# Optimization experiments

Hardware: AMD Instinct MI355X
Metric: run time of the kernel (lower is better)

The kernel has to match this reference:

```python
import jax, jax.numpy as jnp
import numpy as np

B, D, H, E, K = 8192, 1024, 256, 16, 4


def setup_inputs() -> dict:
    key = jax.random.key(0)
    ks = jax.random.split(key, 6)
    s_d = D ** -0.5
    s_h = H ** -0.5
    return {
        "x": jax.random.normal(ks[0], (B, D), dtype=jnp.float32),
        "route_w": jax.random.normal(ks[1], (E, D), dtype=jnp.float32) * s_d,
        "w1": jax.random.normal(ks[2], (E, H, D), dtype=jnp.float32) * s_d,
        "b1": jax.random.normal(ks[3], (E, H), dtype=jnp.float32) * s_d,
        "w2": jax.random.normal(ks[4], (E, D, H), dtype=jnp.float32) * s_h,
        "b2": jax.random.normal(ks[5], (E, D), dtype=jnp.float32) * s_h,
    }


def _moe_forward(x, route_w, w1, b1, w2, b2):
    # Router: logits (B, E) -> top-k softmax weights scattered back to (B, E).
    logits = x @ route_w.T
    top_vals, top_idx = jax.lax.top_k(logits, K)
    top_w = jax.nn.softmax(top_vals, axis=-1)
    rows = jnp.arange(x.shape[0])[:, None]
    weights = jnp.zeros_like(logits).at[rows, top_idx].set(top_w)  # (B, E)

    # Experts: out = sum_e w[:, e] * relu(relu(x W1e^T + b1e) W2e^T + b2e)
    # Non-selected experts have weight 0, so dense-then-weight matches the
    # original masked gather/scatter math exactly (dropout = 0).
    def step(out, params_e):
        W1, bb1, W2, bb2, we = params_e
        h = jax.nn.relu(x @ W1.T + bb1)       # (B, H)
        y = jax.nn.relu(h @ W2.T + bb2)       # (B, D)
        return out + y * we[:, None], None

    out0 = jnp.zeros_like(x)
    out, _ = jax.lax.scan(step, out0, (w1, b1, w2, b2, weights.T))
    return out


def reference(x, route_w, w1, b1, w2, b2):
    return _moe_forward(x, route_w, w1, b1, w2, b2)
```

## Files before the change

### kernel.cpp

```cpp
#include <hip/hip_runtime.h>
#include <stdint.h>

typedef unsigned short u16;
typedef __attribute__((ext_vector_type(8))) short bf16x8;
typedef __attribute__((ext_vector_type(4))) float f32x4;
typedef __attribute__((ext_vector_type(8))) u16 u16x8;
typedef __attribute__((ext_vector_type(4))) u16 u16x4;

#define NTOK 8192
#define DDIM 1024
#define HDIM 256
#define NEXP 16
#define MAXT 272
#define MAXMT (MAXT * 2)
#define MAXSLOT (MAXT * 128)

__device__ __forceinline__ u16 f2bf(float f) {
  uint32_t u = __builtin_bit_cast(uint32_t, f);
  u += 0x7FFFu + ((u >> 16) & 1u);
  return (u16)(u >> 16);
}
__device__ __forceinline__ float bf2f(u16 h) {
  return __builtin_bit_cast(float, (uint32_t)h << 16);
}

__device__ __forceinline__ void gll16(const void* g, void* l) {
  __builtin_amdgcn_global_load_lds((const __attribute__((address_space(1))) void*)g,
                                   (__attribute__((address_space(3))) void*)l,
                                   16, 0, 0);
}

__global__ __launch_bounds__(256) void cvt2_kernel(const float* __restrict__ a,
                                                   const float* __restrict__ b,
                                                   u16* __restrict__ oa,
                                                   u16* __restrict__ ob,
                                                   int nba) {
  const float* in; u16* out;
  int bx = blockIdx.x;
  if (bx < nba) { in = a; out = oa; } else { in = b; out = ob; bx -= nba; }
  size_t i = ((size_t)bx * 256 + threadIdx.x) * 8;
  const float4 p = *(const float4*)(in + i);
  const float4 q = *(const float4*)(in + i + 4);
  u16x8 o;
  o[0] = f2bf(p.x); o[1] = f2bf(p.y); o[2] = f2bf(p.z); o[3] = f2bf(p.w);
  o[4] = f2bf(q.x); o[5] = f2bf(q.y); o[6] = f2bf(q.z); o[7] = f2bf(q.w);
  *(u16x8*)(out + i) = o;
}

__global__ __launch_bounds__(256) void zero_out_kernel(float* __restrict__ p) {
  size_t i = ((size_t)blockIdx.x * 256 + threadIdx.x) * 4;
  *(float4*)(p + i) = (float4){0.f, 0.f, 0.f, 0.f};
}

__global__ __launch_bounds__(256) void router_kernel(const float* __restrict__ x,
                                                     const float* __restrict__ rw,
                                                     int* __restrict__ epack,
                                                     float* __restrict__ ew,
                                                     u16* __restrict__ xbf) {
  __shared__ __align__(16) uint8_t rwlds[65536];
  const int tid = threadIdx.x;

#pragma unroll
  for (int i = 0; i < 16; ++i) {
    int byte = (i * 256 + tid) * 16;
    int sw = byte ^ (((byte >> 8) & 7) << 4);
    *(float4*)(rwlds + sw) = *(const float4*)((const uint8_t*)rw + byte);
  }
  __syncthreads();

  const int lane = tid & 63, wid = tid >> 6;
  const int s = lane & 15;
  const int tok = blockIdx.x * 16 + wid * 4 + (lane >> 4);
  const float* xrow = x + (size_t)tok * DDIM;
  u16* xbrow = xbf + (size_t)tok * DDIM;

  double acc[NEXP];
#pragma unroll
  for (int e = 0; e < NEXP; ++e) acc[e] = 0.0;

#pragma unroll 4
  for (int g = 0; g < 16; ++g) {
    const int d = s * 64 + g * 4;
    float4 xv = *(const float4*)(xrow + d);
    u16x4 o;
    o[0] = f2bf(xv.x); o[1] = f2bf(xv.y); o[2] = f2bf(xv.z); o[3] = f2bf(xv.w);
    *(u16x4*)(xbrow + d) = o;
    const double x0 = xv.x, x1 = xv.y, x2 = xv.z, x3 = xv.w;
    const int roff = (s * 256 + g * 16) ^ ((s & 7) << 4);
#pragma unroll
    for (int e = 0; e < NEXP; ++e) {
      float4 rv = *(const float4*)(rwlds + e * 4096 + roff);
      acc[e] = fma(x0, (double)rv.x, acc[e]);
      acc[e] = fma(x1, (double)rv.y, acc[e]);
      acc[e] = fma(x2, (double)rv.z, acc[e]);
      acc[e] = fma(x3, (double)rv.w, acc[e]);
    }
  }

#define FOLD(H, M)                                                   \
  _Pragma("unroll") for (int i = 0; i < H; ++i) {                    \
    double send = (lane & M) ? acc[i] : acc[i + H];                  \
    double recv = __shfl_xor(send, M);                               \
    acc[i] = ((lane & M) ? acc[i + H] : acc[i]) + recv;              \
  }
  FOLD(8, 1)
  FOLD(4, 2)
  FOLD(2, 4)
  FOLD(1, 8)
#undef FOLD
  const int e_mine = ((lane & 1) << 3) | ((lane & 2) << 1) |
                     ((lane & 4) >> 1) | ((lane & 8) >> 3);

  double val = acc[0];
  double tv[4]; int tidx[4];
#pragma unroll
  for (int k = 0; k < 4; ++k) {
    double bv = val; int be = e_mine;
#pragma unroll
    for (int m = 1; m < 16; m <<= 1) {
      double ov = __shfl_xor(bv, m);
      int oe = __shfl_xor(be, m);
      if (ov > bv || (ov == bv && oe < be)) { bv = ov; be = oe; }
    }
    tv[k] = bv; tidx[k] = be;
    if (e_mine == be) val = -1.0e300;
  }

  if ((lane & 15) == 0) {
    float m0 = (float)tv[0];
    float w[4]; float sum = 0.f;
#pragma unroll
    for (int k = 0; k < 4; ++k) { w[k] = expf((float)tv[k] - m0); sum += w[k]; }
    epack[tok] = tidx[0] | (tidx[1] << 8) | (tidx[2] << 16) | (tidx[3] << 24);
#pragma unroll
    for (int k = 0; k < 4; ++k) ew[tok * 4 + k] = w[k] / sum;
  }
}

__global__ __launch_bounds__(1024) void compact_kernel(const int* __restrict__ epack,
                                                       const float* __restrict__ ew,
                                                       int* __restrict__ texp,
                                                       int* __restrict__ perm,
                                                       float* __restrict__ wsl,
                                                       int* __restrict__ islot) {
  __shared__ int wave_cnt[16][NEXP];
  __shared__ int counts_sm[NEXP];
  __shared__ int wtot[16], wave_off[16];
  const int e = blockIdx.x;
  const int tid = threadIdx.x, lane = tid & 63, w = tid >> 6;

  int ep[8]; unsigned m[8];
#pragma unroll
  for (int j = 0; j < 8; ++j) {
    ep[j] = epack[tid * 8 + j];
    m[j] = (1u << (ep[j] & 255)) | (1u << ((ep[j] >> 8) & 255)) |
           (1u << ((ep[j] >> 16) & 255)) | (1u << ((ep[j] >> 24) & 255));
  }
#pragma unroll
  for (int ee = 0; ee < NEXP; ++ee) {
    int c = 0;
#pragma unroll
    for (int j = 0; j < 8; ++j) c += (m[j] >> ee) & 1u;
#pragma unroll
    for (int off = 32; off > 0; off >>= 1) c += __shfl_xor(c, off);
    if (lane == 0) wave_cnt[w][ee] = c;
  }
  unsigned fm = 0;
#pragma unroll
  for (int j = 0; j < 8; ++j) fm |= ((m[j] >> e) & 1u) << j;
  int s = __popc(fm);
  int incl = s;
#pragma unroll
  for (int d = 1; d < 64; d <<= 1) {
    int t2 = __shfl_up(incl, d);
    if (lane >= d) incl += t2;
  }
  if (lane == 63) wtot[w] = incl;
  __syncthreads();
  if (tid < NEXP) {
    int c = 0;
    for (int w2 = 0; w2 < 16; ++w2) c += wave_cnt[w2][tid];
    counts_sm[tid] = c;
  }
  if (tid == 0) {
    int run = 0;
    for (int w2 = 0; w2 < 16; ++w2) { wave_off[w2] = run; run += wtot[w2]; }
  }
  __syncthreads();
  int base = 0;
  for (int ee = 0; ee < NEXP; ++ee)
    if (ee < e) base += ((counts_sm[ee] + 127) >> 7) << 7;
  int pos = base + wave_off[w] + (incl - s);
#pragma unroll
  for (int j = 0; j < 8; ++j) {
    if ((fm >> j) & 1u) {
      int tok = tid * 8 + j;
      int b0 = ep[j] & 255, b1 = (ep[j] >> 8) & 255, b2_ = (ep[j] >> 16) & 255;
      int k = (b0 == e) ? 0 : ((b1 == e) ? 1 : ((b2_ == e) ? 2 : 3));
      perm[pos] = tok;
      wsl[pos] = ew[tok * 4 + k];
      islot[tok * 4 + k] = pos;
      ++pos;
    }
  }
  int cnt = counts_sm[e];
  int pad = (((cnt + 127) >> 7) << 7) - cnt;
  if (tid < pad) { perm[base + cnt + tid] = 0; wsl[base + cnt + tid] = 0.f; }
  if (e == 0 && tid == 0) {
    int tc = 0;
    for (int ee = 0; ee < NEXP; ++ee) {
      int nt = (counts_sm[ee] + 127) >> 7;
      for (int i = 0; i < nt; ++i) texp[tc++] = ee;
    }
    for (; tc < MAXT; ++tc) texp[tc] = -1;
  }
}

__device__ __forceinline__ void stage128(const u16* __restrict__ base, int ld,
                                         int kbase, uint8_t* dst, int tid) {
#pragma unroll
  for (int i = 0; i < 4; ++i) {
    int u = i * 256 + tid;
    int row = u >> 3, g = u & 7;
    gll16(base + (size_t)row * ld + kbase + ((g ^ (row & 7)) << 3), dst + u * 16);
  }
}
__device__ __forceinline__ void stage64(const u16* __restrict__ base, int ld,
                                        int kbase, uint8_t* dst, int tid) {
#pragma unroll
  for (int i = 0; i < 2; ++i) {
    int u = i * 256 + tid;
    int row = u >> 3, g = u & 7;
    gll16(base + (size_t)row * ld + kbase + ((g ^ (row & 7)) << 3), dst + u * 16);
  }
}
__device__ __forceinline__ void stage_gather64(const u16* __restrict__ xbf,
                                               const int tok[2], int kbase,
                                               uint8_t* dst, int tid) {
#pragma unroll
  for (int i = 0; i < 2; ++i) {
    int u = i * 256 + tid;
    int g = u & 7;
    gll16(xbf + (size_t)tok[i] * DDIM + kbase + ((g ^ ((u >> 3) & 7)) << 3), dst + u * 16);
  }
}

__device__ __forceinline__ void mma64(const uint8_t* Ab, const uint8_t* Bb,
                                      f32x4 acc[2][4], int wm, int wn,
                                      int lrow, int lk) {
#pragma unroll
  for (int s = 0; s < 2; ++s) {
    bf16x8 af[2], bfr[4];
#pragma unroll
    for (int f = 0; f < 2; ++f) {
      int ar = wm * 32 + f * 16 + lrow;
      af[f] = *(const bf16x8*)(Ab + ar * 128 + ((((s << 2) | lk) ^ (ar & 7)) << 4));
    }
#pragma unroll
    for (int f = 0; f < 4; ++f) {
      int br = wn * 64 + f * 16 + lrow;
      bfr[f] = *(const bf16x8*)(Bb + br * 128 + ((((s << 2) | lk) ^ (br & 7)) << 4));
    }
#pragma unroll
    for (int i = 0; i < 2; ++i)
#pragma unroll
      for (int j = 0; j < 4; ++j)
        acc[i][j] = __builtin_amdgcn_mfma_f32_16x16x32_bf16(af[i], bfr[j], acc[i][j], 0, 0, 0);
  }
}

__global__ __launch_bounds__(256) void gemm1_kernel(const u16* __restrict__ xbf,
                                                    const u16* __restrict__ w1bf,
                                                    const float* __restrict__ b1,
                                                    const int* __restrict__ texp,
                                                    const int* __restrict__ perm,
                                                    u16* __restrict__ Hc, int mt0) {
  __shared__ __align__(16) uint8_t smem[2][24576];
  const int mt = mt0 + blockIdx.x;
  const int e = (mt < MAXMT) ? texp[mt >> 1] : -1;
  if (e < 0) return;
  const int n0 = blockIdx.y * 128;
  const int tid = threadIdx.x;
  const int lane = tid & 63, wid = tid >> 6;
  const int wm = wid >> 1, wn = wid & 1;
  const int lrow = lane & 15, lk = lane >> 4;

  int tok[2];
#pragma unroll
  for (int i = 0; i < 2; ++i) tok[i] = perm[mt * 64 + ((i * 256 + tid) >> 3)];
  const u16* Bsrc = w1bf + ((size_t)e * HDIM + n0) * DDIM;

  f32x4 acc[2][4];
#pragma unroll
  for (int i = 0; i < 2; ++i)
#pragma unroll
    for (int j = 0; j < 4; ++j) acc[i][j] = (f32x4){0.f, 0.f, 0.f, 0.f};

  stage_gather64(xbf, tok, 0, smem[0], tid);
  stage128(Bsrc, DDIM, 0, smem[0] + 8192, tid);
  __syncthreads();
  int cur = 0;
  for (int kt = 0; kt < 16; ++kt) {
    if (kt < 15) {
      stage_gather64(xbf, tok, (kt + 1) * 64, smem[cur ^ 1], tid);
      stage128(Bsrc, DDIM, (kt + 1) * 64, smem[cur ^ 1] + 8192, tid);
    }
    mma64(smem[cur], smem[cur] + 8192, acc, wm, wn, lrow, lk);
    __syncthreads();
    cur ^= 1;
  }
#pragma unroll
  for (int j = 0; j < 4; ++j) {
    int n = n0 + wn * 64 + j * 16 + lrow;
    float bias = b1[e * HDIM + n];
#pragma unroll
    for (int i = 0; i < 2; ++i) {
      int rloc = (mt - mt0) * 64 + wm * 32 + i * 16 + lk * 4;
#pragma unroll
      for (int r = 0; r < 4; ++r) {
        float h = fmaxf(acc[i][j][r] + bias, 0.f);
        Hc[((size_t)rloc + r) * HDIM + n] = f2bf(h);
      }
    }
  }
}

__global__ __launch_bounds__(256) void gemm2_main_kernel(const u16* __restrict__ Hc,
                                                         const u16* __restrict__ w2bf,
                                                         const float* __restrict__ b2,
                                                         const int* __restrict__ texp,
                                                         u16* __restrict__ ybuf,
                                                         int nbase, int NC) {
  __shared__ __align__(16) uint8_t smem[2][24576];
  const int mt = blockIdx.x;
  const int e = texp[mt >> 1];
  if (e < 0) return;
  const int nl0 = blockIdx.y * 128;
  const int tid = threadIdx.x;
  const int lane = tid & 63, wid = tid >> 6;
  const int wm = wid >> 1, wn = wid & 1;
  const int lrow = lane & 15, lk = lane >> 4;

  const u16* Asrc = Hc + (size_t)mt * 64 * HDIM;
  const u16* Bsrc = w2bf + ((size_t)e * DDIM + nbase + nl0) * HDIM;

  f32x4 acc[2][4];
#pragma unroll
  for (int i = 0; i < 2; ++i)
#pragma unroll
    for (int j = 0; j < 4; ++j) acc[i][j] = (f32x4){0.f, 0.f, 0.f, 0.f};

  stage64(Asrc, HDIM, 0, smem[0], tid);
  stage128(Bsrc, HDIM, 0, smem[0] + 8192, tid);
  __syncthreads();
  int cur = 0;
  for (int kt = 0; kt < 4; ++kt) {
    if (kt < 3) {
      stage64(Asrc, HDIM, (kt + 1) * 64, smem[cur ^ 1], tid);
      stage128(Bsrc, HDIM, (kt + 1) * 64, smem[cur ^ 1] + 8192, tid);
    }
    mma64(smem[cur], smem[cur] + 8192, acc, wm, wn, lrow, lk);
    __syncthreads();
    cur ^= 1;
  }
  float bias[4];
#pragma unroll
  for (int j = 0; j < 4; ++j)
    bias[j] = b2[e * DDIM + nbase + nl0 + wn * 64 + j * 16 + lrow];
#pragma unroll
  for (int i = 0; i < 2; ++i) {
#pragma unroll
    for (int r = 0; r < 4; ++r) {
      int slot = mt * 64 + wm * 32 + i * 16 + lk * 4 + r;
#pragma unroll
      for (int j = 0; j < 4; ++j) {
        int nloc = nl0 + wn * 64 + j * 16 + lrow;
        float h = fmaxf(acc[i][j][r] + bias[j], 0.f);
        ybuf[(size_t)slot * NC + nloc] = f2bf(h);
      }
    }
  }
}

__global__ __launch_bounds__(256) void gemm2_fb_kernel(const u16* __restrict__ Hc,
                                                       const u16* __restrict__ w2bf,
                                                       const float* __restrict__ b2,
                                                       const int* __restrict__ texp,
                                                       const int* __restrict__ perm,
                                                       const float* __restrict__ wsl,
                                                       float* __restrict__ out, int mt0) {
  __shared__ __align__(16) uint8_t smem[2][24576];
  const int mt = mt0 + blockIdx.x;
  const int e = (mt < MAXMT) ? texp[mt >> 1] : -1;
  if (e < 0) return;
  const int nl0 = blockIdx.y * 128;
  const int tid = threadIdx.x;
  const int lane = tid & 63, wid = tid >> 6;
  const int wm = wid >> 1, wn = wid & 1;
  const int lrow = lane & 15, lk = lane >> 4;

  const u16* Asrc = Hc + (size_t)(mt - mt0) * 64 * HDIM;
  const u16* Bsrc = w2bf + ((size_t)e * DDIM + nl0) * HDIM;

  f32x4 acc[2][4];
#pragma unroll
  for (int i = 0; i < 2; ++i)
#pragma unroll
    for (int j = 0; j < 4; ++j) acc[i][j] = (f32x4){0.f, 0.f, 0.f, 0.f};

  stage64(Asrc, HDIM, 0, smem[0], tid);
  stage128(Bsrc, HDIM, 0, smem[0] + 8192, tid);
  __syncthreads();
  int cur = 0;
  for (int kt = 0; kt < 4; ++kt) {
    if (kt < 3) {
      stage64(Asrc, HDIM, (kt + 1) * 64, smem[cur ^ 1], tid);
      stage128(Bsrc, HDIM, (kt + 1) * 64, smem[cur ^ 1] + 8192, tid);
    }
    mma64(smem[cur], smem[cur] + 8192, acc, wm, wn, lrow, lk);
    __syncthreads();
    cur ^= 1;
  }
  float bias[4];
#pragma unroll
  for (int j = 0; j < 4; ++j)
    bias[j] = b2[e * DDIM + nl0 + wn * 64 + j * 16 + lrow];
#pragma unroll
  for (int i = 0; i < 2; ++i) {
#pragma unroll
    for (int r = 0; r < 4; ++r) {
      int slot = mt * 64 + wm * 32 + i * 16 + lk * 4 + r;
      int tokn = perm[slot];
      float w = wsl[slot];
#pragma unroll
      for (int j = 0; j < 4; ++j) {
        int n = nl0 + wn * 64 + j * 16 + lrow;
        float h = fmaxf(acc[i][j][r] + bias[j], 0.f);
        atomicAdd(&out[(size_t)tokn * DDIM + n], w * h);
      }
    }
  }
}

__global__ __launch_bounds__(256) void combine_kernel(const u16* __restrict__ ybuf,
                                                      const float* __restrict__ ew,
                                                      const int* __restrict__ islot,
                                                      float* __restrict__ out,
                                                      int n0, int NC, int cshift) {
  int gid = blockIdx.x * 256 + threadIdx.x;
  int t = gid >> cshift;
  int c = (gid & ((1 << cshift) - 1)) << 4;
  const int4 sl = *(const int4*)(islot + t * 4);
  const float4 w = *(const float4*)(ew + t * 4);
  float a[16];
#pragma unroll
  for (int k = 0; k < 16; ++k) a[k] = 0.f;
#define ACCROW(SL, W)                                                      \
  {                                                                        \
    u16x8 y0 = *(const u16x8*)(ybuf + (size_t)(SL)*NC + c);                \
    u16x8 y1 = *(const u16x8*)(ybuf + (size_t)(SL)*NC + c + 8);            \
    _Pragma("unroll") for (int k = 0; k < 8; ++k) {                        \
      a[k] += (W)*bf2f(y0[k]); a[8 + k] += (W)*bf2f(y1[k]);                \
    }                                                                      \
  }
  ACCROW(sl.x, w.x); ACCROW(sl.y, w.y); ACCROW(sl.z, w.z); ACCROW(sl.w, w.w);
#undef ACCROW
  float* o = out + (size_t)t * DDIM + n0 + c;
#pragma unroll
  for (int k = 0; k < 16; k += 4)
    *(float4*)(o + k) = (float4){a[k], a[k + 1], a[k + 2], a[k + 3]};
}

extern "C" void kernel_launch(void* const* d_in, const int* in_sizes, int n_in,
                              void* d_out, int out_size, void* d_ws, size_t ws_size,
                              hipStream_t stream) {
  const float* x = (const float*)d_in[0];
  const float* route_w = (const float*)d_in[1];
  const float* w1 = (const float*)d_in[2];
  const float* b1 = (const float*)d_in[3];
  const float* w2 = (const float*)d_in[4];
  const float* b2 = (const float*)d_in[5];
  float* out = (float*)d_out;

  uint8_t* ws = (uint8_t*)d_ws;
  const size_t OFF_EPACK = 0;
  const size_t OFF_EW    = 32768;
  const size_t OFF_ISLOT = 163840;
  const size_t OFF_TEXP  = 294912;
  const size_t OFF_PERM  = 296960;
  const size_t OFF_WSL   = 436224;
  const size_t OFF_X     = 1048576;
  const size_t OFF_W1    = OFF_X + (size_t)NTOK * DDIM * 2;
  const size_t OFF_W2    = OFF_W1 + (size_t)NEXP * HDIM * DDIM * 2;
  const size_t OFF_HC    = OFF_W2 + (size_t)NEXP * DDIM * HDIM * 2;
  const size_t OFF_Y     = OFF_HC + (size_t)MAXSLOT * HDIM * 2;

  int* epack  = (int*)(ws + OFF_EPACK);
  float* ew   = (float*)(ws + OFF_EW);
  int* islot  = (int*)(ws + OFF_ISLOT);
  int* texp   = (int*)(ws + OFF_TEXP);
  int* perm   = (int*)(ws + OFF_PERM);
  float* wsl  = (float*)(ws + OFF_WSL);
  u16* xbf    = (u16*)(ws + OFF_X);
  u16* w1bf   = (u16*)(ws + OFF_W1);
  u16* w2bf   = (u16*)(ws + OFF_W2);
  u16* Hc     = (u16*)(ws + OFF_HC);
  u16* ybuf   = (u16*)(ws + OFF_Y);

  const int nba = (NEXP * HDIM * DDIM) / 2048;
  cvt2_kernel<<<dim3(nba * 2), 256, 0, stream>>>(w1, w2, w1bf, w2bf, nba);
  router_kernel<<<dim3(NTOK / 16), 256, 0, stream>>>(x, route_w, epack, ew, xbf);
  compact_kernel<<<dim3(NEXP), 1024, 0, stream>>>(epack, ew, texp, perm, wsl, islot);

  int ybN = 0;
  for (int cand = 1024; cand >= 128; cand >>= 1) {
    if (ws_size >= OFF_Y + (size_t)MAXSLOT * cand * 2) { ybN = cand; break; }
  }

  if (ybN > 0) {
    gemm1_kernel<<<dim3(MAXMT, HDIM / 128), 256, 0, stream>>>(xbf, w1bf, b1, texp, perm, Hc, 0);
    int cshift = __builtin_ctz(ybN >> 4);
    for (int nb = 0; nb < DDIM; nb += ybN) {
      gemm2_main_kernel<<<dim3(MAXMT, ybN / 128), 256, 0, stream>>>(
          Hc, w2bf, b2, texp, ybuf, nb, ybN);
      combine_kernel<<<dim3((NTOK << cshift) / 256), 256, 0, stream>>>(
          ybuf, ew, islot, out, nb, ybN, cshift);
    }
  } else {
    long room = (long)ws_size - (long)OFF_HC;
    int CT = (int)(room / 65536);
    if (CT > MAXT) CT = MAXT;
    if (CT < 16) CT = 16;
    zero_out_kernel<<<dim3((NTOK * DDIM) / 1024), 256, 0, stream>>>(out);
    for (int t0 = 0; t0 < MAXT; t0 += CT) {
      int ct = (MAXT - t0 < CT) ? (MAXT - t0) : CT;
      gemm1_kernel<<<dim3(ct * 2, HDIM / 128), 256, 0, stream>>>(
          xbf, w1bf, b1, texp, perm, Hc, t0 * 2);
      gemm2_fb_kernel<<<dim3(ct * 2, DDIM / 128), 256, 0, stream>>>(
          Hc, w2bf, b2, texp, perm, wsl, out, t0 * 2);
    }
  }
}
```

Measured before the change: 141.6 us.

## Fuse expert GEMM1 and GEMM2 into one kernel keeping hidden tile in LDS

```diff
diff --git a/kernel.cpp b/kernel.cpp
--- a/kernel.cpp
+++ b/kernel.cpp
@@ -269,6 +269,103 @@
   }
 }
 
+__global__ __launch_bounds__(256) void fused_kernel(const u16* __restrict__ xbf,
+                                                    const u16* __restrict__ w1bf,
+                                                    const u16* __restrict__ w2bf,
+                                                    const float* __restrict__ b1,
+                                                    const float* __restrict__ b2,
+                                                    const int* __restrict__ texp,
+                                                    const int* __restrict__ perm,
+                                                    u16* __restrict__ ybuf, int NC) {
+  __shared__ __align__(16) uint8_t smem[81920];
+  const int mt = blockIdx.x;
+  const int e = texp[mt >> 1];
+  if (e < 0) return;
+  const int tid = threadIdx.x;
+  const int lane = tid & 63, wid = tid >> 6;
+  const int wm = wid >> 1, wn = wid & 1;
+  const int lrow = lane & 15, lk = lane >> 4;
+  uint8_t* stg = smem + 32768;
+
+  int tok[2];
+#pragma unroll
+  for (int i = 0; i < 2; ++i) tok[i] = perm[mt * 64 + ((i * 256 + tid) >> 3)];
+
+  f32x4 acc[2][4];
+#pragma unroll
+  for (int i = 0; i < 2; ++i)
+#pragma unroll
+    for (int j = 0; j < 4; ++j) acc[i][j] = (f32x4){0.f, 0.f, 0.f, 0.f};
+
+  for (int half = 0; half < 2; ++half) {
+    const u16* Bsrc = w1bf + ((size_t)e * HDIM + half * 128) * DDIM;
+    stage_gather64(xbf, tok, 0, stg, tid);
+    stage128(Bsrc, DDIM, 0, stg + 8192, tid);
+    __syncthreads();
+    int cur = 0;
+    for (int kt = 0; kt < 16; ++kt) {
+      if (kt < 15) {
+        stage_gather64(xbf, tok, (kt + 1) * 64, stg + ((cur ^ 1) * 24576), tid);
+        stage128(Bsrc, DDIM, (kt + 1) * 64, stg + ((cur ^ 1) * 24576) + 8192, tid);
+      }
+      mma64(stg + cur * 24576, stg + cur * 24576 + 8192, acc, wm, wn, lrow, lk);
+      __syncthreads();
+      cur ^= 1;
+    }
+#pragma unroll
+    for (int j = 0; j < 4; ++j) {
+      float bias = b1[e * HDIM + half * 128 + wn * 64 + j * 16 + lrow];
+      int g = j * 2 + (lrow >> 3);
+#pragma unroll
+      for (int i = 0; i < 2; ++i) {
+#pragma unroll
+        for (int r = 0; r < 4; ++r) {
+          int row = wm * 32 + i * 16 + lk * 4 + r;
+          float h = fmaxf(acc[i][j][r] + bias, 0.f);
+          int addr = (half * 2 + wn) * 8192 + row * 128 +
+                     ((g ^ (row & 7)) << 4) + (lrow & 7) * 2;
+          *(u16*)(smem + addr) = f2bf(h);
+          acc[i][j][r] = 0.f;
+        }
+      }
+    }
+  }
+  __syncthreads();
+
+  const u16* B2 = w2bf + (size_t)e * DDIM * HDIM;
+  stage128(B2, HDIM, 0, stg, tid);
+  __syncthreads();
+  int cur = 0;
+  for (int s = 0; s < 32; ++s) {
+    const int nb = s >> 2, kt = s & 3;
+    if (s < 31) {
+      const int nb2 = (s + 1) >> 2, kt2 = (s + 1) & 3;
+      stage128(B2 + (size_t)(nb2 * 128) * HDIM, HDIM, kt2 * 64,
+               stg + ((cur ^ 1) << 14), tid);
+    }
+    mma64(smem + kt * 8192, stg + (cur << 14), acc, wm, wn, lrow, lk);
+    if (kt == 3) {
+#pragma unroll
+      for (int j = 0; j < 4; ++j) {
+        float bias = b2[e * DDIM + nb * 128 + wn * 64 + j * 16 + lrow];
+        int nloc = nb * 128 + wn * 64 + j * 16 + lrow;
+#pragma unroll
+        for (int i = 0; i < 2; ++i) {
+#pragma unroll
+          for (int r = 0; r < 4; ++r) {
+            int slot = mt * 64 + wm * 32 + i * 16 + lk * 4 + r;
+            float h = fmaxf(acc[i][j][r] + bias, 0.f);
+            ybuf[(size_t)slot * NC + nloc] = f2bf(h);
+            acc[i][j][r] = 0.f;
+          }
+        }
+      }
+    }
+    __syncthreads();
+    cur ^= 1;
+  }
+}
+
 __global__ __launch_bounds__(256) void gemm1_kernel(const u16* __restrict__ xbf,
                                                     const u16* __restrict__ w1bf,
                                                     const float* __restrict__ b1,
@@ -320,63 +417,6 @@
       for (int r = 0; r < 4; ++r) {
         float h = fmaxf(acc[i][j][r] + bias, 0.f);
         Hc[((size_t)rloc + r) * HDIM + n] = f2bf(h);
-      }
-    }
-  }
-}
-
-__global__ __launch_bounds__(256) void gemm2_main_kernel(const u16* __restrict__ Hc,
-                                                         const u16* __restrict__ w2bf,
-                                                         const float* __restrict__ b2,
-                                                         const int* __restrict__ texp,
-                                                         u16* __restrict__ ybuf,
-                                                         int nbase, int NC) {
-  __shared__ __align__(16) uint8_t smem[2][24576];
-  const int mt = blockIdx.x;
-  const int e = texp[mt >> 1];
-  if (e < 0) return;
-  const int nl0 = blockIdx.y * 128;
-  const int tid = threadIdx.x;
-  const int lane = tid & 63, wid = tid >> 6;
-  const int wm = wid >> 1, wn = wid & 1;
-  const int lrow = lane & 15, lk = lane >> 4;
-
-  const u16* Asrc = Hc + (size_t)mt * 64 * HDIM;
-  const u16* Bsrc = w2bf + ((size_t)e * DDIM + nbase + nl0) * HDIM;
-
-  f32x4 acc[2][4];
-#pragma unroll
-  for (int i = 0; i < 2; ++i)
-#pragma unroll
-    for (int j = 0; j < 4; ++j) acc[i][j] = (f32x4){0.f, 0.f, 0.f, 0.f};
-
-  stage64(Asrc, HDIM, 0, smem[0], tid);
-  stage128(Bsrc, HDIM, 0, smem[0] + 8192, tid);
-  __syncthreads();
-  int cur = 0;
-  for (int kt = 0; kt < 4; ++kt) {
-    if (kt < 3) {
-      stage64(Asrc, HDIM, (kt + 1) * 64, smem[cur ^ 1], tid);
-      stage128(Bsrc, HDIM, (kt + 1) * 64, smem[cur ^ 1] + 8192, tid);
-    }
-    mma64(smem[cur], smem[cur] + 8192, acc, wm, wn, lrow, lk);
-    __syncthreads();
-    cur ^= 1;
-  }
-  float bias[4];
-#pragma unroll
-  for (int j = 0; j < 4; ++j)
-    bias[j] = b2[e * DDIM + nbase + nl0 + wn * 64 + j * 16 + lrow];
-#pragma unroll
-  for (int i = 0; i < 2; ++i) {
-#pragma unroll
-    for (int r = 0; r < 4; ++r) {
-      int slot = mt * 64 + wm * 32 + i * 16 + lk * 4 + r;
-#pragma unroll
-      for (int j = 0; j < 4; ++j) {
-        int nloc = nl0 + wn * 64 + j * 16 + lrow;
-        float h = fmaxf(acc[i][j][r] + bias[j], 0.f);
-        ybuf[(size_t)slot * NC + nloc] = f2bf(h);
       }
     }
   }
@@ -512,20 +552,14 @@
   router_kernel<<<dim3(NTOK / 16), 256, 0, stream>>>(x, route_w, epack, ew, xbf);
   compact_kernel<<<dim3(NEXP), 1024, 0, stream>>>(epack, ew, texp, perm, wsl, islot);
 
-  int ybN = 0;
-  for (int cand = 1024; cand >= 128; cand >>= 1) {
-    if (ws_size >= OFF_Y + (size_t)MAXSLOT * cand * 2) { ybN = cand; break; }
-  }
-
-  if (ybN > 0) {
-    gemm1_kernel<<<dim3(MAXMT, HDIM / 128), 256, 0, stream>>>(xbf, w1bf, b1, texp, perm, Hc, 0);
-    int cshift = __builtin_ctz(ybN >> 4);
-    for (int nb = 0; nb < DDIM; nb += ybN) {
-      gemm2_main_kernel<<<dim3(MAXMT, ybN / 128), 256, 0, stream>>>(
-          Hc, w2bf, b2, texp, ybuf, nb, ybN);
-      combine_kernel<<<dim3((NTOK << cshift) / 256), 256, 0, stream>>>(
-          ybuf, ew, islot, out, nb, ybN, cshift);
-    }
+  const bool full = (ws_size >= OFF_Y + (size_t)MAXSLOT * 1024 * 2);
+
+  if (full) {
+    fused_kernel<<<dim3(MAXMT), 256, 0, stream>>>(xbf, w1bf, w2bf, b1, b2,
+                                                  texp, perm, ybuf, 1024);
+    const int cshift = 6;
+    combine_kernel<<<dim3((NTOK << cshift) / 256), 256, 0, stream>>>(
+        ybuf, ew, islot, out, 0, 1024, cshift);
   } else {
     long room = (long)ws_size - (long)OFF_HC;
     int CT = (int)(room / 65536);
```

After: 161.6 us. 14.1% more time.
